# Kernel tuning notes

Hardware: AMD Instinct MI355X
Metric: run time of the kernel (lower is better)

The kernel has to match this reference:

```python
import jax, jax.numpy as jnp
import numpy as np

B, T, V, H, F = 128, 20, 10000, 512, 49


def _uniform(key, shape, fan):
    s = 1.0 / np.sqrt(fan)
    return jax.random.uniform(key, shape, jnp.float32, -s, s)


def setup_inputs() -> dict:
    key = jax.random.key(0)
    ks = jax.random.split(key, 16)
    return {
        "caption_inputs": jax.random.randint(ks[0], (B, T), 0, V),
        "global_features": jax.random.normal(ks[1], (B, H), jnp.float32),
        "area_features": jax.random.normal(ks[2], (B, H, F), jnp.float32),
        "h0": jnp.zeros((B, H), jnp.float32),
        "c0": jnp.zeros((B, H), jnp.float32),
        # learned params
        "embedding": jax.random.normal(ks[3], (V, H), jnp.float32),
        "W_ih": _uniform(ks[4], (2 * H, 4 * H), H),   # LSTMCell input weights (x @ W_ih)
        "W_hh": _uniform(ks[5], (H, 4 * H), H),
        "b_ih": _uniform(ks[6], (4 * H,), H),
        "b_hh": _uniform(ks[7], (4 * H,), H),
        "Wv": _uniform(ks[8], (H, H), H),             # attention comp_visual
        "Wh": _uniform(ks[9], (H, H), H),             # attention comp_hidden
        "wo": _uniform(ks[10], (H,), H),              # attention output_layer
        "W_out": _uniform(ks[11], (2 * H, V), 2 * H), # decoder output layer
        "b_out": _uniform(ks[12], (V,), 2 * H),
    }


def reference(caption_inputs, global_features, area_features, h0, c0,
              embedding, W_ih, W_hh, b_ih, b_hh, Wv, Wh, wo, W_out, b_out):
    # Precompute attention visual projection (time-invariant): [B,F,H]
    feat = jnp.swapaxes(area_features, 1, 2)          # [B,F,H]
    Vproj = jnp.einsum('bfh,hk->bfk', feat, Wv)       # [B,F,H]
    bias = b_ih + b_hh

    def step(carry, tok):
        h, c = carry
        emb = embedding[tok]                           # [B,H]
        x = jnp.concatenate([emb, global_features], axis=1)   # [B,2H]
        gates = x @ W_ih + h @ W_hh + bias             # [B,4H]
        i, f, g, o = jnp.split(gates, 4, axis=1)
        c = jax.nn.sigmoid(f) * c + jax.nn.sigmoid(i) * jnp.tanh(g)
        h = jax.nn.sigmoid(o) * jnp.tanh(c)
        # spatial attention over F locations
        z = jnp.tanh(Vproj + (h @ Wh)[:, None, :])     # [B,F,H]
        scores = jnp.einsum('bfh,h->bf', z, wo)        # [B,F]
        alpha = jax.nn.softmax(scores, axis=1)
        attended = jnp.einsum('bhf,bf->bh', area_features, alpha)  # [B,H]
        out = jnp.concatenate([h, attended], axis=1) @ W_out + b_out  # [B,V]
        return (h, c), out

    (_, _), outs = jax.lax.scan(step, (h0, c0), caption_inputs.T)  # [T,B,V]
    return jnp.swapaxes(outs, 0, 1)                    # [B,T,V]
```

## Files before the change

kernel.cpp:

```cpp
#include <hip/hip_runtime.h>

#define B_ 128
#define T_ 20
#define V_ 10000
#define H_ 512
#define F_ 49
#define NBLK_ 128

typedef unsigned short u16;
typedef __attribute__((ext_vector_type(8))) short short8;
typedef __attribute__((ext_vector_type(4))) float floatx4;

#define GLOBAL_AS __attribute__((address_space(1)))
#define LDS_AS    __attribute__((address_space(3)))

__device__ inline void load_lds16(const void* g, void* l) {
    __builtin_amdgcn_global_load_lds((const GLOBAL_AS void*)g, (LDS_AS void*)l, 16, 0, 0);
}

__device__ inline u16 f2b(float v) {
    unsigned u = __builtin_bit_cast(unsigned, v);
    unsigned rounding = 0x7FFFu + ((u >> 16) & 1u);
    return (u16)((u + rounding) >> 16);
}
__device__ inline float b2f(u16 h) {
    unsigned u = ((unsigned)h) << 16;
    return __builtin_bit_cast(float, u);
}
__device__ inline float fast_tanh(float x) {
    return 1.f - 2.f / (__expf(2.f * x) + 1.f);
}
__device__ inline float sigm(float x) { return 1.f / (1.f + __expf(-x)); }

__global__ __launch_bounds__(256) void transpose_cvt(const float* __restrict__ src,
                                                     u16* __restrict__ dst, int K, int N) {
    __shared__ float tile[32][33];
    int n0 = blockIdx.x * 32, k0 = blockIdx.y * 32;
    int tx = threadIdx.x, ty = threadIdx.y;
    #pragma unroll
    for (int i = 0; i < 32; i += 8) {
        int k = k0 + ty + i, n = n0 + tx;
        tile[ty + i][tx] = (k < K && n < N) ? src[(size_t)k * N + n] : 0.f;
    }
    __syncthreads();
    #pragma unroll
    for (int i = 0; i < 32; i += 8) {
        int n = n0 + ty + i, k = k0 + tx;
        if (n < N && k < K) dst[(size_t)n * K + k] = f2b(tile[tx][ty + i]);
    }
}

__global__ __launch_bounds__(256) void build_x(const int* __restrict__ cap,
                                               const float* __restrict__ emb,
                                               const float* __restrict__ gf,
                                               u16* __restrict__ X) {
    int r = blockIdx.x;
    int t = r / B_, b = r % B_;
    int tok = cap[b * T_ + t];
    for (int col = threadIdx.x; col < 2 * H_; col += 256) {
        float v = (col < H_) ? emb[(size_t)tok * H_ + col] : gf[(size_t)b * H_ + (col - H_)];
        X[(size_t)r * (2 * H_) + col] = f2b(v);
    }
}

__global__ __launch_bounds__(256) void feat_cvt(const float* __restrict__ area,
                                                u16* __restrict__ feat) {
    int idx = blockIdx.x * 256 + threadIdx.x;
    if (idx >= B_ * F_ * H_) return;
    int h = idx & (H_ - 1);
    int bf_ = idx >> 9;
    int f = bf_ % F_, b = bf_ / F_;
    feat[idx] = f2b(area[((size_t)b * H_ + h) * F_ + f]);
}

__global__ __launch_bounds__(256) void init_hc(const float* __restrict__ h0,
                                               u16* __restrict__ Hall, int* __restrict__ bar) {
    int i = blockIdx.x * 256 + threadIdx.x;
    if (i < B_ * H_) Hall[i] = f2b(h0[i]);
    if (i < 64) bar[i] = 0;
}

__device__ inline void grid_sync(int* bar, int ep) {
    __syncthreads();
    if (threadIdx.x == 0) {
        int old = __hip_atomic_fetch_add(&bar[0], 1, __ATOMIC_ACQ_REL, __HIP_MEMORY_SCOPE_AGENT);
        if (old == NBLK_ - 1) {
            __hip_atomic_store(&bar[0], 0, __ATOMIC_RELAXED, __HIP_MEMORY_SCOPE_AGENT);
            __hip_atomic_store(&bar[32], ep, __ATOMIC_RELEASE, __HIP_MEMORY_SCOPE_AGENT);
        } else {
            while (__hip_atomic_load(&bar[32], __ATOMIC_RELAXED, __HIP_MEMORY_SCOPE_AGENT) < ep)
                __builtin_amdgcn_s_sleep(1);
            (void)__hip_atomic_load(&bar[32], __ATOMIC_ACQUIRE, __HIP_MEMORY_SCOPE_AGENT);
        }
    }
    __syncthreads();
}

__global__ __launch_bounds__(256, 1) void decode_loop(
        const u16* __restrict__ WhhT, const float* __restrict__ Xin,
        const float* __restrict__ c0, u16* __restrict__ Hall,
        u16* __restrict__ Hcat, int* __restrict__ bar) {

    __shared__ __align__(16) u16 Whs[64 * 512];
    __shared__ __align__(16) u16 hstage[32 * 512];
    __shared__ float gl[4 * 32 * 16];
    __shared__ float csh[32 * 16];

    const int tid = threadIdx.x;
    const int wave = tid >> 6, lane = tid & 63;
    const int lm = lane & 15, q = lane >> 4;
    const int bid = blockIdx.x;
    const int jg = bid >> 2, mg = bid & 3;

    #pragma unroll
    for (int i = 0; i < 16; ++i) {
        int row = i * 4 + wave;
        int g = row >> 4, lr = row & 15;
        int grow = g * H_ + jg * 16 + lr;
        load_lds16(WhhT + (size_t)grow * H_ + (size_t)(lane ^ (row & 7)) * 8,
                   (char*)Whs + row * 1024);
    }
    #pragma unroll
    for (int ii = 0; ii < 2; ++ii) {
        int idx = tid + ii * 256;
        int lb = idx >> 4, jj = idx & 15;
        csh[idx] = c0[(size_t)(mg * 32 + lb) * H_ + jg * 16 + jj];
    }

    for (int t = 0; t < T_; ++t) {
        const u16* hprev = Hall + (size_t)t * B_ * H_;
        u16* hnext = Hall + (size_t)(t + 1) * B_ * H_;

        #pragma unroll
        for (int it = 0; it < 8; ++it) {
            int row = it * 4 + wave;
            load_lds16(hprev + (size_t)(mg * 32 + row) * H_ + (size_t)(lane ^ (row & 7)) * 8,
                       (char*)hstage + row * 1024);
        }
        __syncthreads();

        floatx4 acc0 = {0.f, 0.f, 0.f, 0.f}, acc1 = {0.f, 0.f, 0.f, 0.f};
        #pragma unroll
        for (int kt = 0; kt < 16; ++kt) {
            int ch = kt * 4 + q;
            short8 a0 = *(const short8*)&hstage[(lm << 9) + ((ch ^ (lm & 7)) << 3)];
            short8 a1 = *(const short8*)&hstage[((16 + lm) << 9) + ((ch ^ (lm & 7)) << 3)];
            short8 bb = *(const short8*)&Whs[((wave * 16 + lm) << 9) + ((ch ^ (lm & 7)) << 3)];
            acc0 = __builtin_amdgcn_mfma_f32_16x16x32_bf16(a0, bb, acc0, 0, 0, 0);
            acc1 = __builtin_amdgcn_mfma_f32_16x16x32_bf16(a1, bb, acc1, 0, 0, 0);
        }
        #pragma unroll
        for (int r = 0; r < 4; ++r) {
            gl[wave * 512 + (q * 4 + r) * 16 + lm] = acc0[r];
            gl[wave * 512 + (16 + q * 4 + r) * 16 + lm] = acc1[r];
        }
        __syncthreads();

        #pragma unroll
        for (int ii = 0; ii < 2; ++ii) {
            int idx = tid + ii * 256;
            int lb = idx >> 4, jj = idx & 15;
            int grow = mg * 32 + lb, j = jg * 16 + jj;
            const float* xt = Xin + ((size_t)t * B_ + grow) * (4 * H_);
            float gi = gl[0 * 512 + lb * 16 + jj] + xt[j];
            float gf = gl[1 * 512 + lb * 16 + jj] + xt[H_ + j];
            float gg = gl[2 * 512 + lb * 16 + jj] + xt[2 * H_ + j];
            float go = gl[3 * 512 + lb * 16 + jj] + xt[3 * H_ + j];
            float cn = sigm(gf) * csh[idx] + sigm(gi) * fast_tanh(gg);
            csh[idx] = cn;
            u16 hb = f2b(sigm(go) * fast_tanh(cn));
            hnext[(size_t)grow * H_ + j] = hb;
            Hcat[((size_t)grow * T_ + t) * (2 * H_) + j] = hb;
        }

        grid_sync(bar, t + 1);
    }
}

__global__ __launch_bounds__(256) void attn_post(
        const float* __restrict__ ahbuf, const u16* __restrict__ Vprojb,
        const u16* __restrict__ feat, const float* __restrict__ wo,
        u16* __restrict__ Hcat) {
    __shared__ __align__(16) u16 Vsh[F_ * H_];
    __shared__ __align__(16) u16 fsh[F_ * H_];
    __shared__ float ash[H_];
    __shared__ float wosh[H_];
    __shared__ float sc[64];

    const int tid = threadIdx.x;
    const int wave = tid >> 6, lane = tid & 63;
    const int b = blockIdx.x >> 1, th = blockIdx.x & 1;

    const short8* vsrc = (const short8*)(Vprojb + (size_t)b * F_ * H_);
    const short8* fsrc = (const short8*)(feat + (size_t)b * F_ * H_);
    for (int i = tid; i < F_ * H_ / 8; i += 256) {
        ((short8*)Vsh)[i] = vsrc[i];
        ((short8*)fsh)[i] = fsrc[i];
    }
    for (int i = tid; i < H_; i += 256) wosh[i] = wo[i];
    __syncthreads();

    for (int t = th * (T_ / 2); t < (th + 1) * (T_ / 2); ++t) {
        for (int i = tid; i < H_; i += 256)
            ash[i] = ahbuf[((size_t)t * B_ + b) * H_ + i];
        __syncthreads();

        for (int f = wave; f < F_; f += 4) {
            short8 vv = *(const short8*)&Vsh[f * H_ + lane * 8];
            float s = 0.f;
            #pragma unroll
            for (int e = 0; e < 8; ++e) {
                int h = lane * 8 + e;
                s += wosh[h] * fast_tanh(b2f((u16)vv[e]) + ash[h]);
            }
            #pragma unroll
            for (int off = 32; off; off >>= 1) s += __shfl_xor(s, off);
            if (lane == 0) sc[f] = s;
        }
        __syncthreads();

        if (tid < 64) {
            float v = (tid < F_) ? sc[tid] : -1e30f;
            float m = v;
            #pragma unroll
            for (int off = 32; off; off >>= 1) m = fmaxf(m, __shfl_xor(m, off));
            float e = (tid < F_) ? __expf(v - m) : 0.f;
            float sum = e;
            #pragma unroll
            for (int off = 32; off; off >>= 1) sum += __shfl_xor(sum, off);
            if (tid < F_) sc[tid] = e / sum;
        }
        __syncthreads();

        const size_t rowo = ((size_t)b * T_ + t) * (2 * H_);
        for (int h = tid; h < H_; h += 256) {
            float acc = 0.f;
            #pragma unroll
            for (int f = 0; f < F_; ++f) acc += b2f(fsh[f * H_ + h]) * sc[f];
            Hcat[rowo + H_ + h] = f2b(acc);
        }
        __syncthreads();
    }
}

template <int WRITE_BF16>
__global__ __launch_bounds__(256) void gemm2(const u16* __restrict__ A, int lda,
                                             const u16* __restrict__ Bt, int ldb,
                                             void* __restrict__ Cout, int ldc,
                                             const float* __restrict__ bias1,
                                             const float* __restrict__ bias2,
                                             int M, int N, int K) {
    __shared__ __align__(16) u16 As[128 * 32];
    __shared__ __align__(16) u16 Bs[128 * 32];
    const int tid = threadIdx.x, wave = tid >> 6, lane = tid & 63;
    const int wr = wave >> 1, wc = wave & 1;
    const int lm = lane & 15, q = lane >> 4;
    const int m0 = blockIdx.x * 128, n0 = blockIdx.y * 128;

    const int off = wave * 1024 + lane * 16;
    const int r0 = off >> 6;
    const int c0 = (off & 63) >> 1;

    const u16* gA0 = A + (size_t)(m0 + r0) * lda + c0;
    const u16* gA1 = A + (size_t)(m0 + r0 + 64) * lda + c0;
    int nb0 = n0 + r0;      if (nb0 > N - 1) nb0 = N - 1;
    int nb1 = n0 + r0 + 64; if (nb1 > N - 1) nb1 = N - 1;
    const u16* gB0 = Bt + (size_t)nb0 * ldb + c0;
    const u16* gB1 = Bt + (size_t)nb1 * ldb + c0;
    char* lA0 = (char*)As + wave * 1024;
    char* lA1 = (char*)As + 4096 + wave * 1024;
    char* lB0 = (char*)Bs + wave * 1024;
    char* lB1 = (char*)Bs + 4096 + wave * 1024;

    floatx4 acc[4][4];
    #pragma unroll
    for (int i = 0; i < 4; ++i)
        #pragma unroll
        for (int j = 0; j < 4; ++j) acc[i][j] = floatx4{0.f, 0.f, 0.f, 0.f};

    const int nkt = K >> 5;
    for (int kt = 0; kt < nkt; ++kt) {
        const int ko = kt * 32;
        load_lds16(gA0 + ko, lA0);
        load_lds16(gA1 + ko, lA1);
        load_lds16(gB0 + ko, lB0);
        load_lds16(gB1 + ko, lB1);
        __syncthreads();
        short8 af[4], bf[4];
        #pragma unroll
        for (int i = 0; i < 4; ++i)
            af[i] = *(const short8*)&As[(wr * 64 + i * 16 + lm) * 32 + q * 8];
        #pragma unroll
        for (int j = 0; j < 4; ++j)
            bf[j] = *(const short8*)&Bs[(wc * 64 + j * 16 + lm) * 32 + q * 8];
        #pragma unroll
        for (int i = 0; i < 4; ++i)
            #pragma unroll
            for (int j = 0; j < 4; ++j)
                acc[i][j] = __builtin_amdgcn_mfma_f32_16x16x32_bf16(af[i], bf[j], acc[i][j], 0, 0, 0);
        __syncthreads();
    }

    #pragma unroll
    for (int i = 0; i < 4; ++i) {
        const int row = m0 + wr * 64 + i * 16 + q * 4;
        #pragma unroll
        for (int j = 0; j < 4; ++j) {
            const int col = n0 + wc * 64 + j * 16 + lm;
            if (col < N) {
                #pragma unroll
                for (int r = 0; r < 4; ++r) {
                    float v = acc[i][j][r];
                    if (bias1) v += bias1[col];
                    if (bias2) v += bias2[col];
                    if (WRITE_BF16) ((u16*)Cout)[(size_t)(row + r) * ldc + col] = f2b(v);
                    else            ((float*)Cout)[(size_t)(row + r) * ldc + col] = v;
                }
            }
        }
    }
}

extern "C" void kernel_launch(void* const* d_in, const int* in_sizes, int n_in,
                              void* d_out, int out_size, void* d_ws, size_t ws_size,
                              hipStream_t stream) {
    const int*   cap   = (const int*)d_in[0];
    const float* gf    = (const float*)d_in[1];
    const float* area  = (const float*)d_in[2];
    const float* h0    = (const float*)d_in[3];
    const float* c0    = (const float*)d_in[4];
    const float* emb   = (const float*)d_in[5];
    const float* W_ih  = (const float*)d_in[6];
    const float* W_hh  = (const float*)d_in[7];
    const float* b_ih  = (const float*)d_in[8];
    const float* b_hh  = (const float*)d_in[9];
    const float* Wv    = (const float*)d_in[10];
    const float* Wh    = (const float*)d_in[11];
    const float* wo    = (const float*)d_in[12];
    const float* W_out = (const float*)d_in[13];
    const float* b_out = (const float*)d_in[14];
    float* out = (float*)d_out;

    char* p = (char*)d_ws;
    auto alloc = [&](size_t bytes) {
        char* q = p;
        p += (bytes + 255) & ~(size_t)255;
        return q;
    };
    u16*   X      = (u16*)alloc((size_t)T_ * B_ * 2 * H_ * 2);
    u16*   WihT   = (u16*)alloc((size_t)4 * H_ * 2 * H_ * 2);
    u16*   WhhT   = (u16*)alloc((size_t)4 * H_ * H_ * 2);
    u16*   WvT    = (u16*)alloc((size_t)H_ * H_ * 2);
    u16*   WhT    = (u16*)alloc((size_t)H_ * H_ * 2);
    u16*   WoutT  = (u16*)alloc((size_t)V_ * 2 * H_ * 2);
    u16*   feat   = (u16*)alloc((size_t)B_ * F_ * H_ * 2);
    float* Xin    = (float*)alloc((size_t)T_ * B_ * 4 * H_ * 4);
    u16*   Vprojb = (u16*)alloc((size_t)B_ * F_ * H_ * 2);
    float* ahbuf  = (float*)alloc((size_t)T_ * B_ * H_ * 4);
    u16*   Hall   = (u16*)alloc((size_t)(T_ + 1) * B_ * H_ * 2);
    int*   bar    = (int*)alloc(256);
    u16*   Hcat   = (u16*)alloc((size_t)B_ * T_ * 2 * H_ * 2);

    dim3 tb(32, 8);
    transpose_cvt<<<dim3(4 * H_ / 32, 2 * H_ / 32), tb, 0, stream>>>(W_ih, WihT, 2 * H_, 4 * H_);
    transpose_cvt<<<dim3(4 * H_ / 32, H_ / 32), tb, 0, stream>>>(W_hh, WhhT, H_, 4 * H_);
    transpose_cvt<<<dim3(H_ / 32, H_ / 32), tb, 0, stream>>>(Wv, WvT, H_, H_);
    transpose_cvt<<<dim3(H_ / 32, H_ / 32), tb, 0, stream>>>(Wh, WhT, H_, H_);
    transpose_cvt<<<dim3((V_ + 31) / 32, 2 * H_ / 32), tb, 0, stream>>>(W_out, WoutT, 2 * H_, V_);
    build_x<<<T_ * B_, 256, 0, stream>>>(cap, emb, gf, X);
    feat_cvt<<<(B_ * F_ * H_ + 255) / 256, 256, 0, stream>>>(area, feat);
    init_hc<<<(B_ * H_ + 255) / 256, 256, 0, stream>>>(h0, Hall, bar);

    gemm2<0><<<dim3(T_ * B_ / 128, 4 * H_ / 128), 256, 0, stream>>>(
        X, 2 * H_, WihT, 2 * H_, Xin, 4 * H_, b_ih, b_hh, T_ * B_, 4 * H_, 2 * H_);
    gemm2<1><<<dim3(B_ * F_ / 128, H_ / 128), 256, 0, stream>>>(
        feat, H_, WvT, H_, Vprojb, H_, nullptr, nullptr, B_ * F_, H_, H_);

    decode_loop<<<NBLK_, 256, 0, stream>>>(WhhT, Xin, c0, Hall, Hcat, bar);

    gemm2<0><<<dim3(T_ * B_ / 128, H_ / 128), 256, 0, stream>>>(
        Hall + (size_t)B_ * H_, H_, WhT, H_, ahbuf, H_, nullptr, nullptr, T_ * B_, H_, H_);

    attn_post<<<2 * B_, 256, 0, stream>>>(ahbuf, Vprojb, feat, wo, Hcat);

    gemm2<0><<<dim3(T_ * B_ / 128, (V_ + 127) / 128), 256, 0, stream>>>(
        Hcat, 2 * H_, WoutT, 2 * H_, out, V_, b_out, nullptr, T_ * B_, V_, 2 * H_);
}
```

Baseline: 666.3 us.

## Split decode grid barrier per batch group and move Hcat copy to attention

Replaces the single 128-block grid barrier with four independent barriers, one per batch group (mg). Each group's 32 blocks synchronise only with each other, using a monotonic counter with no reset. This relies on each group reading only its own batch rows of h. The scattered Hcat write is also removed from the serial decode loop, and attn_post copies h rows from Hall into Hcat with vector loads instead. The aim is to cut barrier contention and latency on the critical recurrent path, at the cost of an extra copy in attn_post.

Measured after the change: 652.6 us. 2.1% less time.

```diff
diff --git a/kernel.cpp b/kernel.cpp
--- a/kernel.cpp
+++ b/kernel.cpp
@@ -77,21 +77,18 @@
                                                u16* __restrict__ Hall, int* __restrict__ bar) {
     int i = blockIdx.x * 256 + threadIdx.x;
     if (i < B_ * H_) Hall[i] = f2b(h0[i]);
-    if (i < 64) bar[i] = 0;
-}
-
-__device__ inline void grid_sync(int* bar, int ep) {
+    if (i < 256) bar[i] = 0;
+}
+
+__device__ inline void grid_sync_mg(int* base, int ep) {
     __syncthreads();
     if (threadIdx.x == 0) {
-        int old = __hip_atomic_fetch_add(&bar[0], 1, __ATOMIC_ACQ_REL, __HIP_MEMORY_SCOPE_AGENT);
-        if (old == NBLK_ - 1) {
-            __hip_atomic_store(&bar[0], 0, __ATOMIC_RELAXED, __HIP_MEMORY_SCOPE_AGENT);
-            __hip_atomic_store(&bar[32], ep, __ATOMIC_RELEASE, __HIP_MEMORY_SCOPE_AGENT);
-        } else {
-            while (__hip_atomic_load(&bar[32], __ATOMIC_RELAXED, __HIP_MEMORY_SCOPE_AGENT) < ep)
-                __builtin_amdgcn_s_sleep(1);
-            (void)__hip_atomic_load(&bar[32], __ATOMIC_ACQUIRE, __HIP_MEMORY_SCOPE_AGENT);
-        }
+        int old = __hip_atomic_fetch_add(&base[0], 1, __ATOMIC_ACQ_REL, __HIP_MEMORY_SCOPE_AGENT);
+        if (old == ep * 32 - 1)
+            __hip_atomic_store(&base[32], ep, __ATOMIC_RELEASE, __HIP_MEMORY_SCOPE_AGENT);
+        while (__hip_atomic_load(&base[32], __ATOMIC_RELAXED, __HIP_MEMORY_SCOPE_AGENT) < ep)
+            __builtin_amdgcn_s_sleep(2);
+        (void)__hip_atomic_load(&base[32], __ATOMIC_ACQUIRE, __HIP_MEMORY_SCOPE_AGENT);
     }
     __syncthreads();
 }
@@ -99,7 +96,7 @@
 __global__ __launch_bounds__(256, 1) void decode_loop(
         const u16* __restrict__ WhhT, const float* __restrict__ Xin,
         const float* __restrict__ c0, u16* __restrict__ Hall,
-        u16* __restrict__ Hcat, int* __restrict__ bar) {
+        int* __restrict__ bar) {
 
     __shared__ __align__(16) u16 Whs[64 * 512];
     __shared__ __align__(16) u16 hstage[32 * 512];
@@ -111,6 +108,7 @@
     const int lm = lane & 15, q = lane >> 4;
     const int bid = blockIdx.x;
     const int jg = bid >> 2, mg = bid & 3;
+    int* mybar = bar + mg * 64;
 
     #pragma unroll
     for (int i = 0; i < 16; ++i) {
@@ -168,19 +166,17 @@
             float go = gl[3 * 512 + lb * 16 + jj] + xt[3 * H_ + j];
             float cn = sigm(gf) * csh[idx] + sigm(gi) * fast_tanh(gg);
             csh[idx] = cn;
-            u16 hb = f2b(sigm(go) * fast_tanh(cn));
-            hnext[(size_t)grow * H_ + j] = hb;
-            Hcat[((size_t)grow * T_ + t) * (2 * H_) + j] = hb;
-        }
-
-        grid_sync(bar, t + 1);
+            hnext[(size_t)grow * H_ + j] = f2b(sigm(go) * fast_tanh(cn));
+        }
+
+        grid_sync_mg(mybar, t + 1);
     }
 }
 
 __global__ __launch_bounds__(256) void attn_post(
         const float* __restrict__ ahbuf, const u16* __restrict__ Vprojb,
         const u16* __restrict__ feat, const float* __restrict__ wo,
-        u16* __restrict__ Hcat) {
+        const u16* __restrict__ Hall, u16* __restrict__ Hcat) {
     __shared__ __align__(16) u16 Vsh[F_ * H_];
     __shared__ __align__(16) u16 fsh[F_ * H_];
     __shared__ float ash[H_];
@@ -233,6 +229,9 @@
         __syncthreads();
 
         const size_t rowo = ((size_t)b * T_ + t) * (2 * H_);
+        const short8* hrow = (const short8*)(Hall + ((size_t)(t + 1) * B_ + b) * H_);
+        for (int i = tid; i < H_ / 8; i += 256)
+            ((short8*)(Hcat + rowo))[i] = hrow[i];
         for (int h = tid; h < H_; h += 256) {
             float acc = 0.f;
             #pragma unroll
@@ -358,7 +357,7 @@
     u16*   Vprojb = (u16*)alloc((size_t)B_ * F_ * H_ * 2);
     float* ahbuf  = (float*)alloc((size_t)T_ * B_ * H_ * 4);
     u16*   Hall   = (u16*)alloc((size_t)(T_ + 1) * B_ * H_ * 2);
-    int*   bar    = (int*)alloc(256);
+    int*   bar    = (int*)alloc(1024);
     u16*   Hcat   = (u16*)alloc((size_t)B_ * T_ * 2 * H_ * 2);
 
     dim3 tb(32, 8);
@@ -376,12 +375,12 @@
     gemm2<1><<<dim3(B_ * F_ / 128, H_ / 128), 256, 0, stream>>>(
         feat, H_, WvT, H_, Vprojb, H_, nullptr, nullptr, B_ * F_, H_, H_);
 
-    decode_loop<<<NBLK_, 256, 0, stream>>>(WhhT, Xin, c0, Hall, Hcat, bar);
+    decode_loop<<<NBLK_, 256, 0, stream>>>(WhhT, Xin, c0, Hall, bar);
 
     gemm2<0><<<dim3(T_ * B_ / 128, H_ / 128), 256, 0, stream>>>(
         Hall + (size_t)B_ * H_, H_, WhT, H_, ahbuf, H_, nullptr, nullptr, T_ * B_, H_, H_);
 
-    attn_post<<<2 * B_, 256, 0, stream>>>(ahbuf, Vprojb, feat, wo, Hcat);
+    attn_post<<<2 * B_, 256, 0, stream>>>(ahbuf, Vprojb, feat, wo, Hall, Hcat);
 
     gemm2<0><<<dim3(T_ * B_ / 128, (V_ + 127) / 128), 256, 0, stream>>>(
         Hcat, 2 * H_, WoutT, 2 * H_, out, V_, b_out, nullptr, T_ * B_, V_, 2 * H_);
```
